# Kernel optimization log

Measured on AMD Instinct MI355X. Metric: run time of the kernel, lower is better.

The kernel has to match this reference:

```python
import jax, jax.numpy as jnp
import numpy as np

N_FEATURE = 128
N_OUTPUT = 2  # number of GatedEquivariant layers
N_ATOMS = 100000
N_GRAPHS = 128


def setup_inputs() -> dict:
    key = jax.random.key(0)
    ks = jax.random.split(key, 16)
    F = N_FEATURE
    L = N_OUTPUT
    sc = 1.0 / np.sqrt(F)
    s = jax.random.normal(ks[0], (1, N_ATOMS, F), dtype=jnp.float32)
    v = jax.random.normal(ks[1], (1, N_ATOMS, 3, F), dtype=jnp.float32)
    r = jax.random.normal(ks[2], (1, N_ATOMS, 3), dtype=jnp.float32)
    # one-hot batch mask: each atom belongs to one of N_GRAPHS molecules
    seg = jnp.sort(jax.random.randint(ks[3], (N_ATOMS,), 0, N_GRAPHS))
    batch_mask = (seg[None, :] == jnp.arange(N_GRAPHS)[:, None]).astype(jnp.float32)[..., None]  # (B,N,1)
    # GatedEquivariant params, stacked over L layers; stored (in,out) so y = x @ W + b
    w1 = jax.random.normal(ks[4], (L, F, F), dtype=jnp.float32) * sc
    w2 = jax.random.normal(ks[5], (L, F, F), dtype=jnp.float32) * sc
    a1w = jax.random.normal(ks[6], (L, 2 * F, F), dtype=jnp.float32) * (1.0 / np.sqrt(2 * F))
    a1b = jnp.zeros((L, F), dtype=jnp.float32)
    a2w = jax.random.normal(ks[7], (L, F, 2 * F), dtype=jnp.float32) * sc
    a2b = jnp.zeros((L, 2 * F), dtype=jnp.float32)
    out_w = jax.random.normal(ks[8], (F, 1), dtype=jnp.float32) * sc
    out_b = jnp.zeros((1,), dtype=jnp.float32)
    return {"s": s, "v": v, "r": r, "batch_mask": batch_mask,
            "w1": w1, "w2": w2, "a1w": a1w, "a1b": a1b,
            "a2w": a2w, "a2b": a2b, "out_w": out_w, "out_b": out_b}


def _gated_equivariant(s, v, w1, w2, a1w, a1b, a2w, a2b):
    # v: (1,N,3,F); linear layers act on the feature (last) dim
    v1 = jnp.einsum('bncf,fg->bncg', v, w1)
    v2 = jnp.einsum('bncf,fg->bncg', v, w2)
    n2 = jnp.linalg.norm(v2, axis=-2)                 # (1,N,F) norm over spatial dim
    h = jnp.concatenate([s, n2], axis=-1)             # (1,N,2F)
    h = jax.nn.silu(h @ a1w + a1b)                    # (1,N,F)
    h = h @ a2w + a2b                                 # (1,N,2F)
    s_out, g = jnp.split(h, 2, axis=-1)
    v_out = g[..., None, :] * v1                      # gate broadcast over spatial dim
    return s_out, v_out


def reference(s, v, r, batch_mask, w1, w2, a1w, a1b, a2w, a2b, out_w, out_b):
    del r  # r only used when dy=True (not the case here)
    for i in range(w1.shape[0]):  # small fixed layer count
        s, v = _gated_equivariant(s, v, w1[i], w2[i], a1w[i], a1b[i], a2w[i], a2b[i])
    sc = s @ out_w + out_b                            # (1,N,1)
    # torch: (sc.repeat(B,1,1) * batch_mask).sum(-2) == masked segment-sum via broadcast
    y = jnp.sum(sc * batch_mask, axis=-2)             # (B,1)
    return y
```

## Files before the change

### kernel.cpp

```cpp
#include <hip/hip_runtime.h>
#include <hip/hip_bf16.h>

#define NF 128
#define NF2 256
#define NATOMS 100000
#define NGRAPH 128

#define MT 32
#define NBLK (NATOMS/MT)
#define NTHR 512

#define OW1 0
#define OW2 16384
#define OA1 32768
#define OA2 65536
#define LAYER_SZ 98304

typedef __attribute__((ext_vector_type(8))) short bf16x8;
typedef __attribute__((ext_vector_type(4))) short bf16x4;
typedef __attribute__((ext_vector_type(4))) float f32x4;

static __device__ __forceinline__ float bf2f(__hip_bfloat16 x) { return __bfloat162float(x); }
static __device__ __forceinline__ __hip_bfloat16 f2bf(float x) { return __float2bfloat16(x); }
static __device__ __forceinline__ unsigned short f2bfu(float x) {
  __hip_bfloat16 h = __float2bfloat16(x);
  return *(unsigned short*)&h;
}
static __device__ __forceinline__ bf16x8 pack8(float4 lo, float4 hi) {
  union { unsigned short s[8]; bf16x8 v; } u;
  u.s[0]=f2bfu(lo.x); u.s[1]=f2bfu(lo.y); u.s[2]=f2bfu(lo.z); u.s[3]=f2bfu(lo.w);
  u.s[4]=f2bfu(hi.x); u.s[5]=f2bfu(hi.y); u.s[6]=f2bfu(hi.z); u.s[7]=f2bfu(hi.w);
  return u.v;
}
static __device__ __forceinline__ bf16x4 pack4f(f32x4 a) {
  union { unsigned short s[4]; bf16x4 v; } u;
  u.s[0]=f2bfu(a[0]); u.s[1]=f2bfu(a[1]); u.s[2]=f2bfu(a[2]); u.s[3]=f2bfu(a[3]);
  return u.v;
}
static __device__ __forceinline__ float bfs2f(short s) {
  __hip_bfloat16 h; *(short*)&h = s; return __bfloat162float(h);
}

static __device__ __forceinline__ bf16x8 ldfrag(const __hip_bfloat16* buf, int gr, int row, int gi) {
  return *(const bf16x8*)&buf[(row*gr + (gi ^ (row & 7)))*8];
}
static __device__ __forceinline__ void stq(__hip_bfloat16* buf, int gr, int row, int colb, bf16x4 v) {
  int gi = colb >> 3, off = colb & 7;
  *(bf16x4*)&buf[(row*gr + (gi ^ (row & 7)))*8 + off] = v;
}

__global__ __launch_bounds__(256)
void prep_weights(const float* __restrict__ w1, const float* __restrict__ w2,
                  const float* __restrict__ a1w, const float* __restrict__ a2w,
                  __hip_bfloat16* __restrict__ blob) {
  int gid = blockIdx.x * 256 + threadIdx.x;
  int layer = gid / 12288;
  int r = gid - layer * 12288;
  const float* W; int N, nks, g; __hip_bfloat16* dst;
  if (r < 2048)      { W = w1  + layer*NF*NF;  N = NF;  nks = 4; dst = blob + layer*LAYER_SZ + OW1; g = r; }
  else if (r < 4096) { W = w2  + layer*NF*NF;  N = NF;  nks = 4; dst = blob + layer*LAYER_SZ + OW2; g = r - 2048; }
  else if (r < 8192) { W = a1w + layer*NF2*NF; N = NF;  nks = 8; dst = blob + layer*LAYER_SZ + OA1; g = r - 4096; }
  else               { W = a2w + layer*NF*NF2; N = NF2; nks = 4; dst = blob + layer*LAYER_SZ + OA2; g = r - 8192; }
  int lane = g & 63;
  int ks = (g >> 6) % nks;
  int ct = g / (64 * nks);
  int k0 = ks * 32 + ((lane >> 4) << 3);
  int n  = ct * 16 + (lane & 15);
  __hip_bfloat16* o = dst + (size_t)((ct * nks + ks) * 64 + lane) * 8;
  #pragma unroll
  for (int j = 0; j < 8; ++j) o[j] = f2bf(W[(size_t)(k0 + j) * N + n]);
}

__global__ __launch_bounds__(NTHR, 4)
void fused_equiv(const float* __restrict__ s_g, const float* __restrict__ v_g,
                 const __hip_bfloat16* __restrict__ blob,
                 const float* __restrict__ a1b, const float* __restrict__ a2b,
                 const float* __restrict__ out_w, const float* __restrict__ out_b,
                 float* __restrict__ sc) {
  __shared__ __hip_bfloat16 vcur[3*MT*NF];
  __shared__ __hip_bfloat16 hbuf[MT*NF2];
  __shared__ __hip_bfloat16 h1[MT*NF];

  const int tid  = threadIdx.x;
  const int wave = tid >> 6;
  const int lane = tid & 63;
  const int l15  = lane & 15;
  const int quad = lane >> 4;
  const int a0   = blockIdx.x * MT;
  const int fb   = wave*16 + quad*4;

  {
    int row = tid >> 4, gi = tid & 15;
    const float* sp = s_g + (size_t)a0*NF + row*NF + gi*8;
    float4 lo = *(const float4*)sp;
    float4 hi = *(const float4*)(sp + 4);
    *(bf16x8*)&hbuf[(row*32 + (gi ^ (row & 7)))*8] = pack8(lo, hi);
    #pragma unroll
    for (int u = 0; u < 3; ++u) {
      int g = tid + u*512;
      int R = g >> 4, gi2 = g & 15;
      int at = R / 3, c = R - 3*at;
      const float* vp = v_g + (size_t)a0*3*NF + R*NF + gi2*8;
      float4 vlo = *(const float4*)vp;
      float4 vhi = *(const float4*)(vp + 4);
      *(bf16x8*)&vcur[((c*MT + at)*16 + (gi2 ^ (at & 7)))*8] = pack8(vlo, vhi);
    }
  }
  __syncthreads();

  {
    const __hip_bfloat16* lb = blob;
    bf16x8 wf[4];
    #pragma unroll
    for (int ks = 0; ks < 4; ++ks)
      wf[ks] = *(const bf16x8*)&lb[OW2 + ((size_t)(wave*4 + ks)*64 + lane)*8];
    #pragma unroll
    for (int rt = 0; rt < 2; ++rt) {
      int arow = rt*16 + l15;
      f32x4 nq = {0.f,0.f,0.f,0.f};
      #pragma unroll
      for (int c = 0; c < 3; ++c) {
        f32x4 acc = {0.f,0.f,0.f,0.f};
        #pragma unroll
        for (int ks = 0; ks < 4; ++ks) {
          bf16x8 af = ldfrag(vcur + c*MT*NF, 16, arow, ks*4 + quad);
          acc = __builtin_amdgcn_mfma_f32_16x16x32_bf16(wf[ks], af, acc, 0, 0, 0);
        }
        #pragma unroll
        for (int i = 0; i < 4; ++i) nq[i] += acc[i]*acc[i];
      }
      f32x4 nv;
      #pragma unroll
      for (int i = 0; i < 4; ++i) nv[i] = sqrtf(nq[i]);
      stq(hbuf, 32, arow, NF + fb, pack4f(nv));
    }
  }
  __syncthreads();

  {
    const __hip_bfloat16* lb = blob;
    bf16x8 a1f[8];
    #pragma unroll
    for (int ks = 0; ks < 8; ++ks)
      a1f[ks] = *(const bf16x8*)&lb[OA1 + ((size_t)(wave*8 + ks)*64 + lane)*8];
    const f32x4 b1a4 = *(const f32x4*)&a1b[fb];
    #pragma unroll
    for (int rt = 0; rt < 2; ++rt) {
      int arow = rt*16 + l15;
      f32x4 acc = {0.f,0.f,0.f,0.f};
      #pragma unroll
      for (int ks = 0; ks < 8; ++ks) {
        bf16x8 af = ldfrag(hbuf, 32, arow, ks*4 + quad);
        acc = __builtin_amdgcn_mfma_f32_16x16x32_bf16(a1f[ks], af, acc, 0, 0, 0);
      }
      f32x4 h;
      #pragma unroll
      for (int i = 0; i < 4; ++i) {
        float x = acc[i] + b1a4[i];
        h[i] = x / (1.0f + __expf(-x));
      }
      stq(h1, 16, arow, fb, pack4f(h));
    }
  }
  __syncthreads();

  f32x4 g[2];
  {
    const __hip_bfloat16* lb = blob;
    {
      bf16x8 asf[4];
      #pragma unroll
      for (int ks = 0; ks < 4; ++ks)
        asf[ks] = *(const bf16x8*)&lb[OA2 + ((size_t)(wave*4 + ks)*64 + lane)*8];
      const f32x4 b2s4 = *(const f32x4*)&a2b[fb];
      #pragma unroll
      for (int rt = 0; rt < 2; ++rt) {
        int arow = rt*16 + l15;
        f32x4 hs = {0.f,0.f,0.f,0.f};
        #pragma unroll
        for (int ks = 0; ks < 4; ++ks) {
          bf16x8 af = ldfrag(h1, 16, arow, ks*4 + quad);
          hs = __builtin_amdgcn_mfma_f32_16x16x32_bf16(asf[ks], af, hs, 0, 0, 0);
        }
        f32x4 sv;
        #pragma unroll
        for (int i = 0; i < 4; ++i) sv[i] = hs[i] + b2s4[i];
        stq(hbuf, 32, arow, fb, pack4f(sv));
      }
    }
    {
      bf16x8 agf[4];
      #pragma unroll
      for (int ks = 0; ks < 4; ++ks)
        agf[ks] = *(const bf16x8*)&lb[OA2 + ((size_t)((wave+8)*4 + ks)*64 + lane)*8];
      const f32x4 b2g4 = *(const f32x4*)&a2b[NF + fb];
      #pragma unroll
      for (int rt = 0; rt < 2; ++rt) {
        int arow = rt*16 + l15;
        f32x4 hg = {0.f,0.f,0.f,0.f};
        #pragma unroll
        for (int ks = 0; ks < 4; ++ks) {
          bf16x8 af = ldfrag(h1, 16, arow, ks*4 + quad);
          hg = __builtin_amdgcn_mfma_f32_16x16x32_bf16(agf[ks], af, hg, 0, 0, 0);
        }
        #pragma unroll
        for (int i = 0; i < 4; ++i) g[rt][i] = hg[i] + b2g4[i];
      }
    }
  }

  {
    const __hip_bfloat16* lb = blob;
    bf16x8 wf[4];
    #pragma unroll
    for (int ks = 0; ks < 4; ++ks)
      wf[ks] = *(const bf16x8*)&lb[OW1 + ((size_t)(wave*4 + ks)*64 + lane)*8];
    #pragma unroll
    for (int c = 0; c < 3; ++c) {
      f32x4 acc0 = {0.f,0.f,0.f,0.f}, acc1 = {0.f,0.f,0.f,0.f};
      #pragma unroll
      for (int ks = 0; ks < 4; ++ks) {
        bf16x8 af0 = ldfrag(vcur + c*MT*NF, 16, l15,      ks*4 + quad);
        bf16x8 af1 = ldfrag(vcur + c*MT*NF, 16, 16 + l15, ks*4 + quad);
        acc0 = __builtin_amdgcn_mfma_f32_16x16x32_bf16(wf[ks], af0, acc0, 0, 0, 0);
        acc1 = __builtin_amdgcn_mfma_f32_16x16x32_bf16(wf[ks], af1, acc1, 0, 0, 0);
      }
      __syncthreads();
      f32x4 gv0, gv1;
      #pragma unroll
      for (int i = 0; i < 4; ++i) { gv0[i] = g[0][i]*acc0[i]; gv1[i] = g[1][i]*acc1[i]; }
      stq(vcur + c*MT*NF, 16, l15,      fb, pack4f(gv0));
      stq(vcur + c*MT*NF, 16, 16 + l15, fb, pack4f(gv1));
    }
  }
  __syncthreads();

  {
    const __hip_bfloat16* lb = blob + LAYER_SZ;
    bf16x8 wf[4];
    #pragma unroll
    for (int ks = 0; ks < 4; ++ks)
      wf[ks] = *(const bf16x8*)&lb[OW2 + ((size_t)(wave*4 + ks)*64 + lane)*8];
    #pragma unroll
    for (int rt = 0; rt < 2; ++rt) {
      int arow = rt*16 + l15;
      f32x4 nq = {0.f,0.f,0.f,0.f};
      #pragma unroll
      for (int c = 0; c < 3; ++c) {
        f32x4 acc = {0.f,0.f,0.f,0.f};
        #pragma unroll
        for (int ks = 0; ks < 4; ++ks) {
          bf16x8 af = ldfrag(vcur + c*MT*NF, 16, arow, ks*4 + quad);
          acc = __builtin_amdgcn_mfma_f32_16x16x32_bf16(wf[ks], af, acc, 0, 0, 0);
        }
        #pragma unroll
        for (int i = 0; i < 4; ++i) nq[i] += acc[i]*acc[i];
      }
      f32x4 nv;
      #pragma unroll
      for (int i = 0; i < 4; ++i) nv[i] = sqrtf(nq[i]);
      stq(hbuf, 32, arow, NF + fb, pack4f(nv));
    }
  }
  __syncthreads();

  {
    const __hip_bfloat16* lb = blob + LAYER_SZ;
    bf16x8 a1f[8];
    #pragma unroll
    for (int ks = 0; ks < 8; ++ks)
      a1f[ks] = *(const bf16x8*)&lb[OA1 + ((size_t)(wave*8 + ks)*64 + lane)*8];
    const f32x4 b1g4 = *(const f32x4*)&a1b[NF + fb];
    #pragma unroll
    for (int rt = 0; rt < 2; ++rt) {
      int arow = rt*16 + l15;
      f32x4 acc = {0.f,0.f,0.f,0.f};
      #pragma unroll
      for (int ks = 0; ks < 8; ++ks) {
        bf16x8 af = ldfrag(hbuf, 32, arow, ks*4 + quad);
        acc = __builtin_amdgcn_mfma_f32_16x16x32_bf16(a1f[ks], af, acc, 0, 0, 0);
      }
      f32x4 h;
      #pragma unroll
      for (int i = 0; i < 4; ++i) {
        float x = acc[i] + b1g4[i];
        h[i] = x / (1.0f + __expf(-x));
      }
      stq(h1, 16, arow, fb, pack4f(h));
    }
  }
  __syncthreads();

  {
    const __hip_bfloat16* lb = blob + LAYER_SZ;
    bf16x8 asf[4];
    #pragma unroll
    for (int ks = 0; ks < 4; ++ks)
      asf[ks] = *(const bf16x8*)&lb[OA2 + ((size_t)(wave*4 + ks)*64 + lane)*8];
    const f32x4 b2s24 = *(const f32x4*)&a2b[2*NF + fb];
    #pragma unroll
    for (int rt = 0; rt < 2; ++rt) {
      int arow = rt*16 + l15;
      f32x4 hs = {0.f,0.f,0.f,0.f};
      #pragma unroll
      for (int ks = 0; ks < 4; ++ks) {
        bf16x8 af = ldfrag(h1, 16, arow, ks*4 + quad);
        hs = __builtin_amdgcn_mfma_f32_16x16x32_bf16(asf[ks], af, hs, 0, 0, 0);
      }
      f32x4 sv;
      #pragma unroll
      for (int i = 0; i < 4; ++i) sv[i] = hs[i] + b2s24[i];
      stq(hbuf, 32, arow, fb, pack4f(sv));
    }
  }
  __syncthreads();

  {
    int a   = tid >> 4;
    int sub = tid & 15;
    bf16x8 sv = ldfrag(hbuf, 32, a, sub);
    const float* owp = out_w + sub*8;
    float p = 0.f;
    #pragma unroll
    for (int j = 0; j < 8; ++j) p += bfs2f(sv[j]) * owp[j];
    p += __shfl_down(p, 8, 16);
    p += __shfl_down(p, 4, 16);
    p += __shfl_down(p, 2, 16);
    p += __shfl_down(p, 1, 16);
    if (sub == 0) sc[a0 + a] = p + out_b[0];
  }
}

#define CHUNK 6256
__global__ __launch_bounds__(256)
void reduce_partial(const float* __restrict__ mask, const float* __restrict__ sc,
                    float* __restrict__ partial) {
  int b  = blockIdx.x >> 4;
  int ch = blockIdx.x & 15;
  int n0 = ch * CHUNK;
  int n1 = n0 + CHUNK; if (n1 > NATOMS) n1 = NATOMS;
  const float4* m4 = (const float4*)(mask + (size_t)b * NATOMS + n0);
  const float4* s4 = (const float4*)(sc + n0);
  int nq = (n1 - n0) >> 2;
  float acc = 0.f;
  for (int i = threadIdx.x; i < nq; i += 256) {
    float4 m = m4[i], s = s4[i];
    acc += m.x*s.x + m.y*s.y + m.z*s.z + m.w*s.w;
  }
  #pragma unroll
  for (int d = 32; d > 0; d >>= 1) acc += __shfl_down(acc, d, 64);
  __shared__ float red[4];
  if ((threadIdx.x & 63) == 0) red[threadIdx.x >> 6] = acc;
  __syncthreads();
  if (threadIdx.x == 0) partial[blockIdx.x] = red[0] + red[1] + red[2] + red[3];
}

__global__ void reduce_final(const float* __restrict__ partial, float* __restrict__ out) {
  int b = threadIdx.x;
  if (b < NGRAPH) {
    float s = 0.f;
    #pragma unroll
    for (int k = 0; k < 16; ++k) s += partial[b*16 + k];
    out[b] = s;
  }
}

extern "C" void kernel_launch(void* const* d_in, const int* in_sizes, int n_in,
                              void* d_out, int out_size, void* d_ws, size_t ws_size,
                              hipStream_t stream) {
  const float* s    = (const float*)d_in[0];
  const float* v    = (const float*)d_in[1];
  const float* mask = (const float*)d_in[3];
  const float* w1   = (const float*)d_in[4];
  const float* w2   = (const float*)d_in[5];
  const float* a1w  = (const float*)d_in[6];
  const float* a1b  = (const float*)d_in[7];
  const float* a2w  = (const float*)d_in[8];
  const float* a2b  = (const float*)d_in[9];
  const float* outw = (const float*)d_in[10];
  const float* outb = (const float*)d_in[11];

  char* ws = (char*)d_ws;
  __hip_bfloat16* blob = (__hip_bfloat16*)ws;
  float* sc      = (float*)(ws + (size_t)2*LAYER_SZ*2);
  float* partial = (float*)(ws + (size_t)2*LAYER_SZ*2 + NATOMS*4);

  prep_weights<<<96, 256, 0, stream>>>(w1, w2, a1w, a2w, blob);
  fused_equiv<<<NBLK, NTHR, 0, stream>>>(s, v, blob, a1b, a2b, outw, outb, sc);
  reduce_partial<<<NGRAPH*16, 256, 0, stream>>>(mask, sc, partial);
  reduce_final<<<1, 128, 0, stream>>>(partial, (float*)d_out);
}
```

Before: 355.3 us.

## Double atom tile to 64 with 1024 threads and drop separate h1 buffer

Raises the per-block atom tile from 32 to 64 and the block from 512 to 1024 threads (16 waves, two row groups of 8 column tiles). The SiLU hidden activations are now written into the upper half of hbuf behind an extra barrier, so the separate h1 LDS buffer is removed. Bounds checks handle the ragged last tile. The aim is to amortise per-block weight-fragment loads and launch overhead over more atoms while keeping LDS per block near the old size. The cost is extra barriers and 1024-thread blocks, which may limit occupancy and latency hiding.

Result: slower. 413.1 us (+16.3%).

```diff
diff --git a/kernel.cpp b/kernel.cpp
--- a/kernel.cpp
+++ b/kernel.cpp
@@ -6,9 +6,9 @@
 #define NATOMS 100000
 #define NGRAPH 128
 
-#define MT 32
-#define NBLK (NATOMS/MT)
-#define NTHR 512
+#define MT 64
+#define NBLK ((NATOMS + MT - 1) / MT)
+#define NTHR 1024
 
 #define OW1 0
 #define OW2 16384
@@ -79,7 +79,6 @@
                  float* __restrict__ sc) {
   __shared__ __hip_bfloat16 vcur[3*MT*NF];
   __shared__ __hip_bfloat16 hbuf[MT*NF2];
-  __shared__ __hip_bfloat16 h1[MT*NF];
 
   const int tid  = threadIdx.x;
   const int wave = tid >> 6;
@@ -87,22 +86,33 @@
   const int l15  = lane & 15;
   const int quad = lane >> 4;
   const int a0   = blockIdx.x * MT;
-  const int fb   = wave*16 + quad*4;
-
-  {
+  const int ct   = wave & 7;
+  const int rtb  = (wave >> 3) * 2;
+  const int fb   = ct*16 + quad*4;
+  const int ar0  = rtb*16 + l15;
+  const int ar1  = ar0 + 16;
+
+  {
+    const float4 z4 = {0.f,0.f,0.f,0.f};
     int row = tid >> 4, gi = tid & 15;
-    const float* sp = s_g + (size_t)a0*NF + row*NF + gi*8;
-    float4 lo = *(const float4*)sp;
-    float4 hi = *(const float4*)(sp + 4);
+    float4 lo = z4, hi = z4;
+    if (a0 + row < NATOMS) {
+      const float* sp = s_g + (size_t)(a0+row)*NF + gi*8;
+      lo = *(const float4*)sp;
+      hi = *(const float4*)(sp + 4);
+    }
     *(bf16x8*)&hbuf[(row*32 + (gi ^ (row & 7)))*8] = pack8(lo, hi);
     #pragma unroll
     for (int u = 0; u < 3; ++u) {
-      int g = tid + u*512;
+      int g = tid + u*1024;
       int R = g >> 4, gi2 = g & 15;
       int at = R / 3, c = R - 3*at;
-      const float* vp = v_g + (size_t)a0*3*NF + R*NF + gi2*8;
-      float4 vlo = *(const float4*)vp;
-      float4 vhi = *(const float4*)(vp + 4);
+      float4 vlo = z4, vhi = z4;
+      if (a0 + at < NATOMS) {
+        const float* vp = v_g + (size_t)(a0+at)*3*NF + (size_t)c*NF + gi2*8;
+        vlo = *(const float4*)vp;
+        vhi = *(const float4*)(vp + 4);
+      }
       *(bf16x8*)&vcur[((c*MT + at)*16 + (gi2 ^ (at & 7)))*8] = pack8(vlo, vhi);
     }
   }
@@ -113,10 +123,10 @@
     bf16x8 wf[4];
     #pragma unroll
     for (int ks = 0; ks < 4; ++ks)
-      wf[ks] = *(const bf16x8*)&lb[OW2 + ((size_t)(wave*4 + ks)*64 + lane)*8];
+      wf[ks] = *(const bf16x8*)&lb[OW2 + ((size_t)(ct*4 + ks)*64 + lane)*8];
     #pragma unroll
     for (int rt = 0; rt < 2; ++rt) {
-      int arow = rt*16 + l15;
+      int arow = rt ? ar1 : ar0;
       f32x4 nq = {0.f,0.f,0.f,0.f};
       #pragma unroll
       for (int c = 0; c < 3; ++c) {
@@ -142,25 +152,27 @@
     bf16x8 a1f[8];
     #pragma unroll
     for (int ks = 0; ks < 8; ++ks)
-      a1f[ks] = *(const bf16x8*)&lb[OA1 + ((size_t)(wave*8 + ks)*64 + lane)*8];
+      a1f[ks] = *(const bf16x8*)&lb[OA1 + ((size_t)(ct*8 + ks)*64 + lane)*8];
     const f32x4 b1a4 = *(const f32x4*)&a1b[fb];
+    f32x4 h[2];
     #pragma unroll
     for (int rt = 0; rt < 2; ++rt) {
-      int arow = rt*16 + l15;
+      int arow = rt ? ar1 : ar0;
       f32x4 acc = {0.f,0.f,0.f,0.f};
       #pragma unroll
       for (int ks = 0; ks < 8; ++ks) {
         bf16x8 af = ldfrag(hbuf, 32, arow, ks*4 + quad);
         acc = __builtin_amdgcn_mfma_f32_16x16x32_bf16(a1f[ks], af, acc, 0, 0, 0);
       }
-      f32x4 h;
       #pragma unroll
       for (int i = 0; i < 4; ++i) {
         float x = acc[i] + b1a4[i];
-        h[i] = x / (1.0f + __expf(-x));
-      }
-      stq(h1, 16, arow, fb, pack4f(h));
-    }
+        h[rt][i] = x / (1.0f + __expf(-x));
+      }
+    }
+    __syncthreads();
+    stq(hbuf, 32, ar0, NF + fb, pack4f(h[0]));
+    stq(hbuf, 32, ar1, NF + fb, pack4f(h[1]));
   }
   __syncthreads();
 
@@ -171,15 +183,15 @@
       bf16x8 asf[4];
       #pragma unroll
       for (int ks = 0; ks < 4; ++ks)
-        asf[ks] = *(const bf16x8*)&lb[OA2 + ((size_t)(wave*4 + ks)*64 + lane)*8];
+        asf[ks] = *(const bf16x8*)&lb[OA2 + ((size_t)(ct*4 + ks)*64 + lane)*8];
       const f32x4 b2s4 = *(const f32x4*)&a2b[fb];
       #pragma unroll
       for (int rt = 0; rt < 2; ++rt) {
-        int arow = rt*16 + l15;
+        int arow = rt ? ar1 : ar0;
         f32x4 hs = {0.f,0.f,0.f,0.f};
         #pragma unroll
         for (int ks = 0; ks < 4; ++ks) {
-          bf16x8 af = ldfrag(h1, 16, arow, ks*4 + quad);
+          bf16x8 af = ldfrag(hbuf, 32, arow, 16 + ks*4 + quad);
           hs = __builtin_amdgcn_mfma_f32_16x16x32_bf16(asf[ks], af, hs, 0, 0, 0);
         }
         f32x4 sv;
@@ -192,15 +204,15 @@
       bf16x8 agf[4];
       #pragma unroll
       for (int ks = 0; ks < 4; ++ks)
-        agf[ks] = *(const bf16x8*)&lb[OA2 + ((size_t)((wave+8)*4 + ks)*64 + lane)*8];
+        agf[ks] = *(const bf16x8*)&lb[OA2 + ((size_t)((ct+8)*4 + ks)*64 + lane)*8];
       const f32x4 b2g4 = *(const f32x4*)&a2b[NF + fb];
       #pragma unroll
       for (int rt = 0; rt < 2; ++rt) {
-        int arow = rt*16 + l15;
+        int arow = rt ? ar1 : ar0;
         f32x4 hg = {0.f,0.f,0.f,0.f};
         #pragma unroll
         for (int ks = 0; ks < 4; ++ks) {
-          bf16x8 af = ldfrag(h1, 16, arow, ks*4 + quad);
+          bf16x8 af = ldfrag(hbuf, 32, arow, 16 + ks*4 + quad);
           hg = __builtin_amdgcn_mfma_f32_16x16x32_bf16(agf[ks], af, hg, 0, 0, 0);
         }
         #pragma unroll
@@ -214,14 +226,14 @@
     bf16x8 wf[4];
     #pragma unroll
     for (int ks = 0; ks < 4; ++ks)
-      wf[ks] = *(const bf16x8*)&lb[OW1 + ((size_t)(wave*4 + ks)*64 + lane)*8];
+      wf[ks] = *(const bf16x8*)&lb[OW1 + ((size_t)(ct*4 + ks)*64 + lane)*8];
     #pragma unroll
     for (int c = 0; c < 3; ++c) {
       f32x4 acc0 = {0.f,0.f,0.f,0.f}, acc1 = {0.f,0.f,0.f,0.f};
       #pragma unroll
       for (int ks = 0; ks < 4; ++ks) {
-        bf16x8 af0 = ldfrag(vcur + c*MT*NF, 16, l15,      ks*4 + quad);
-        bf16x8 af1 = ldfrag(vcur + c*MT*NF, 16, 16 + l15, ks*4 + quad);
+        bf16x8 af0 = ldfrag(vcur + c*MT*NF, 16, ar0, ks*4 + quad);
+        bf16x8 af1 = ldfrag(vcur + c*MT*NF, 16, ar1, ks*4 + quad);
         acc0 = __builtin_amdgcn_mfma_f32_16x16x32_bf16(wf[ks], af0, acc0, 0, 0, 0);
         acc1 = __builtin_amdgcn_mfma_f32_16x16x32_bf16(wf[ks], af1, acc1, 0, 0, 0);
       }
@@ -229,8 +241,8 @@
       f32x4 gv0, gv1;
       #pragma unroll
       for (int i = 0; i < 4; ++i) { gv0[i] = g[0][i]*acc0[i]; gv1[i] = g[1][i]*acc1[i]; }
-      stq(vcur + c*MT*NF, 16, l15,      fb, pack4f(gv0));
-      stq(vcur + c*MT*NF, 16, 16 + l15, fb, pack4f(gv1));
+      stq(vcur + c*MT*NF, 16, ar0, fb, pack4f(gv0));
+      stq(vcur + c*MT*NF, 16, ar1, fb, pack4f(gv1));
     }
   }
   __syncthreads();
@@ -240,10 +252,10 @@
     bf16x8 wf[4];
     #pragma unroll
     for (int ks = 0; ks < 4; ++ks)
-      wf[ks] = *(const bf16x8*)&lb[OW2 + ((size_t)(wave*4 + ks)*64 + lane)*8];
+      wf[ks] = *(const bf16x8*)&lb[OW2 + ((size_t)(ct*4 + ks)*64 + lane)*8];
     #pragma unroll
     for (int rt = 0; rt < 2; ++rt) {
-      int arow = rt*16 + l15;
+      int arow = rt ? ar1 : ar0;
       f32x4 nq = {0.f,0.f,0.f,0.f};
       #pragma unroll
       for (int c = 0; c < 3; ++c) {
@@ -269,25 +281,27 @@
     bf16x8 a1f[8];
     #pragma unroll
     for (int ks = 0; ks < 8; ++ks)
-      a1f[ks] = *(const bf16x8*)&lb[OA1 + ((size_t)(wave*8 + ks)*64 + lane)*8];
+      a1f[ks] = *(const bf16x8*)&lb[OA1 + ((size_t)(ct*8 + ks)*64 + lane)*8];
     const f32x4 b1g4 = *(const f32x4*)&a1b[NF + fb];
+    f32x4 h[2];
     #pragma unroll
     for (int rt = 0; rt < 2; ++rt) {
-      int arow = rt*16 + l15;
+      int arow = rt ? ar1 : ar0;
       f32x4 acc = {0.f,0.f,0.f,0.f};
       #pragma unroll
       for (int ks = 0; ks < 8; ++ks) {
         bf16x8 af = ldfrag(hbuf, 32, arow, ks*4 + quad);
         acc = __builtin_amdgcn_mfma_f32_16x16x32_bf16(a1f[ks], af, acc, 0, 0, 0);
       }
-      f32x4 h;
       #pragma unroll
       for (int i = 0; i < 4; ++i) {
         float x = acc[i] + b1g4[i];
-        h[i] = x / (1.0f + __expf(-x));
-      }
-      stq(h1, 16, arow, fb, pack4f(h));
-    }
+        h[rt][i] = x / (1.0f + __expf(-x));
+      }
+    }
+    __syncthreads();
+    stq(hbuf, 32, ar0, NF + fb, pack4f(h[0]));
+    stq(hbuf, 32, ar1, NF + fb, pack4f(h[1]));
   }
   __syncthreads();
 
@@ -296,15 +310,15 @@
     bf16x8 asf[4];
     #pragma unroll
     for (int ks = 0; ks < 4; ++ks)
-      asf[ks] = *(const bf16x8*)&lb[OA2 + ((size_t)(wave*4 + ks)*64 + lane)*8];
+      asf[ks] = *(const bf16x8*)&lb[OA2 + ((size_t)(ct*4 + ks)*64 + lane)*8];
     const f32x4 b2s24 = *(const f32x4*)&a2b[2*NF + fb];
     #pragma unroll
     for (int rt = 0; rt < 2; ++rt) {
-      int arow = rt*16 + l15;
+      int arow = rt ? ar1 : ar0;
       f32x4 hs = {0.f,0.f,0.f,0.f};
       #pragma unroll
       for (int ks = 0; ks < 4; ++ks) {
-        bf16x8 af = ldfrag(h1, 16, arow, ks*4 + quad);
+        bf16x8 af = ldfrag(hbuf, 32, arow, 16 + ks*4 + quad);
         hs = __builtin_amdgcn_mfma_f32_16x16x32_bf16(asf[ks], af, hs, 0, 0, 0);
       }
       f32x4 sv;
@@ -327,7 +341,7 @@
     p += __shfl_down(p, 4, 16);
     p += __shfl_down(p, 2, 16);
     p += __shfl_down(p, 1, 16);
-    if (sub == 0) sc[a0 + a] = p + out_b[0];
+    if (sub == 0 && a0 + a < NATOMS) sc[a0 + a] = p + out_b[0];
   }
 }
 
```
